# Performance work log

Hardware: AMD Instinct MI355X
Metric: run time of the kernel (lower is better)

The kernel has to match this reference:

```python
import jax, jax.numpy as jnp
import numpy as np

EPS = 1e-5
NHEADS = 4
NLAYERS = 6

def layernorm(x, g, b):
    m = jnp.mean(x, axis=-1, keepdims=True)
    v = jnp.var(x, axis=-1, keepdims=True)
    return (x - m) * jax.lax.rsqrt(v + EPS) * g + b

def leaky_relu(x):
    return jnp.where(x >= 0, x, 0.1 * x)  # LeakyReLU(negative_slope=0.1)

def biased_mha(x, bias, mask, Wq, bq, Wk, bk, Wv, bv, Wo, bo):
    # dgl.nn.BiasedMHA: scores = (q/sqrt(dh)) k^T + bias (per-head), mask==True -> -inf
    B, N, D = x.shape
    dh = D // NHEADS
    q = (x @ Wq + bq).reshape(B, N, NHEADS, dh) * (dh ** -0.5)
    k = (x @ Wk + bk).reshape(B, N, NHEADS, dh)
    v = (x @ Wv + bv).reshape(B, N, NHEADS, dh)
    scores = jnp.einsum('bqhd,bkhd->bqkh', q, k) + bias  # [B,N,N,H]
    scores = jnp.where(mask[..., None], -jnp.inf, scores)
    w = jax.nn.softmax(scores, axis=2)  # softmax over keys
    out = jnp.einsum('bqkh,bkhd->bqhd', w, v).reshape(B, N, D)
    return out @ Wo + bo

def graphormer_forward(node_feat_new, attn_bias, deg_in_emb, deg_out_emb,
                       mlp_n_W1, mlp_n_b1, mlp_n_W2, mlp_n_b2,
                       Wq, bq, Wk, bk, Wv, bv, Wo, bo,
                       ln1_g, ln1_b, W1, b1, W2, b2, ln2_g, ln2_b,
                       mlp_out_W1, mlp_out_b1, mlp_out_W2, mlp_out_b2,
                       in_degree, out_degree, attn_mask, po_idx):
    # DegreeEncoder (directed): clamp to max_degree=8, sum of two embedding tables
    deg = deg_in_emb[jnp.clip(in_degree, 0, 8)] + deg_out_emb[jnp.clip(out_degree, 0, 8)]
    # mlp_n: Linear -> LeakyReLU(0.1) -> Linear
    h = leaky_relu(node_feat_new @ mlp_n_W1 + mlp_n_b1) @ mlp_n_W2 + mlp_n_b2
    x = h + deg
    mask = attn_mask != 0
    for i in range(NLAYERS):  # 6 GraphormerLayers, norm_first=False (post-norm)
        res = x
        a = biased_mha(x, attn_bias, mask, Wq[i], bq[i], Wk[i], bk[i], Wv[i], bv[i], Wo[i], bo[i])
        x = layernorm(res + a, ln1_g[i], ln1_b[i])
        res = x
        f = jax.nn.relu(x @ W1[i] + b1[i]) @ W2[i] + b2[i]  # FFN with ReLU
        x = layernorm(res + f, ln2_g[i], ln2_b[i])
    B = x.shape[0]
    sel = x[jnp.arange(B)[:, None], po_idx].reshape(-1, x.shape[-1])  # gather PO nodes
    return leaky_relu(sel @ mlp_out_W1 + mlp_out_b1) @ mlp_out_W2 + mlp_out_b2

def setup_inputs():
    B, N, F_IN, D, HID, P, L = 8, 1024, 64, 512, 1024, 128, 6
    key = jax.random.key(0)
    ks = jax.random.split(key, 32)
    def w(k, shape, fan_in):
        return jax.random.normal(k, shape, jnp.float32) / np.float32(np.sqrt(fan_in))
    return dict(
        node_feat_new=jax.random.normal(ks[0], (B, N, F_IN), jnp.float32),
        in_degree=jax.random.randint(ks[1], (B, N), 0, 9),
        out_degree=jax.random.randint(ks[2], (B, N), 0, 9),
        dist=jax.random.randint(ks[3], (B, N, N), 0, 6).astype(jnp.int32),
        attn_mask=jax.random.randint(ks[4], (B, N, N), 0, 2).astype(jnp.int32),
        po_idx=jax.random.randint(ks[5], (B, P), 0, N),
        attn_bias=jax.random.uniform(ks[6], (B, N, N, NHEADS), jnp.float32),
        deg_in_emb=w(ks[7], (9, D), D),
        deg_out_emb=w(ks[8], (9, D), D),
        mlp_n_W1=w(ks[9], (F_IN, D // 2), F_IN), mlp_n_b1=jnp.zeros((D // 2,), jnp.float32),
        mlp_n_W2=w(ks[10], (D // 2, D), D // 2), mlp_n_b2=jnp.zeros((D,), jnp.float32),
        Wq=w(ks[11], (L, D, D), D), bq=jnp.zeros((L, D), jnp.float32),
        Wk=w(ks[12], (L, D, D), D), bk=jnp.zeros((L, D), jnp.float32),
        Wv=w(ks[13], (L, D, D), D), bv=jnp.zeros((L, D), jnp.float32),
        Wo=w(ks[14], (L, D, D), D), bo=jnp.zeros((L, D), jnp.float32),
        ln1_g=jnp.ones((L, D), jnp.float32), ln1_b=jnp.zeros((L, D), jnp.float32),
        W1=w(ks[15], (L, D, HID), D), b1=jnp.zeros((L, HID), jnp.float32),
        W2=w(ks[16], (L, HID, D), HID), b2=jnp.zeros((L, D), jnp.float32),
        ln2_g=jnp.ones((L, D), jnp.float32), ln2_b=jnp.zeros((L, D), jnp.float32),
        mlp_out_W1=w(ks[17], (D, D // 2), D), mlp_out_b1=jnp.zeros((D // 2,), jnp.float32),
        mlp_out_W2=w(ks[18], (D // 2, 1), D // 2), mlp_out_b2=jnp.zeros((1,), jnp.float32),
    )

def reference(node_feat_new, in_degree, out_degree, dist, attn_mask, po_idx, attn_bias,
              deg_in_emb, deg_out_emb, mlp_n_W1, mlp_n_b1, mlp_n_W2, mlp_n_b2,
              Wq, bq, Wk, bk, Wv, bv, Wo, bo, ln1_g, ln1_b, W1, b1, W2, b2, ln2_g, ln2_b,
              mlp_out_W1, mlp_out_b1, mlp_out_W2, mlp_out_b2):
    del dist  # original computes spatial encoding from dist but overwrites attn_bias with rand (dead code)
    return graphormer_forward(node_feat_new, attn_bias, deg_in_emb, deg_out_emb,
                              mlp_n_W1, mlp_n_b1, mlp_n_W2, mlp_n_b2,
                              Wq, bq, Wk, bk, Wv, bv, Wo, bo,
                              ln1_g, ln1_b, W1, b1, W2, b2, ln2_g, ln2_b,
                              mlp_out_W1, mlp_out_b1, mlp_out_W2, mlp_out_b2,
                              in_degree, out_degree, attn_mask, po_idx)
```

## Files before the change

kernel.cpp:

```cpp
#include <hip/hip_runtime.h>

typedef unsigned short u16;
typedef unsigned int u32;
typedef short bf16x8 __attribute__((ext_vector_type(8)));
typedef float f32x4 __attribute__((ext_vector_type(4)));

__device__ __forceinline__ float us2f(u16 u) {
  union { unsigned int i; float f; } x; x.i = ((unsigned int)u) << 16; return x.f;
}
__device__ __forceinline__ u16 f2bf(float f) {
  union { float f; unsigned int i; } x; x.f = f;
  unsigned int i = x.i;
  return (u16)((i + 0x7FFFu + ((i >> 16) & 1u)) >> 16);
}
__device__ __forceinline__ int probe_f32(const void* p) {
  return ((const u16*)p)[0] == 0;
}
__device__ __forceinline__ float ldf(const void* p, size_t i, int f32) {
  return f32 ? ((const float*)p)[i] : us2f(((const u16*)p)[i]);
}
__device__ __forceinline__ float4 ldf4(const void* p, size_t i, int f32) {
  if (f32) return *(const float4*)((const float*)p + i);
  const ushort4 t = *(const ushort4*)((const u16*)p + i);
  return make_float4(us2f(t.x), us2f(t.y), us2f(t.z), us2f(t.w));
}

__device__ __forceinline__ void tconv(u16 (*t)[72], const void* W, size_t off,
    int K, int N, u16* dst, int k0, int n0, int f32, int tid) {
  const int rr = tid >> 2, rc = (tid & 3) * 16;
  const size_t src = off + (size_t)(k0 + rr) * N + n0 + rc;
  u16 tmp[16];
  if (f32) {
    const float* p = (const float*)W + src;
#pragma unroll
    for (int q = 0; q < 4; q++) {
      const float4 f = *(const float4*)(p + q * 4);
      tmp[q * 4 + 0] = f2bf(f.x); tmp[q * 4 + 1] = f2bf(f.y);
      tmp[q * 4 + 2] = f2bf(f.z); tmp[q * 4 + 3] = f2bf(f.w);
    }
  } else {
    const u16* p = (const u16*)W + src;
    *(bf16x8*)&tmp[0] = *(const bf16x8*)p;
    *(bf16x8*)&tmp[8] = *(const bf16x8*)(p + 8);
  }
#pragma unroll
  for (int j = 0; j < 16; j++) t[rr][rc + j] = tmp[j];
  __syncthreads();
  const int wr = tid >> 2, wc = (tid & 3) * 16;
  u16 ot[16];
#pragma unroll
  for (int j = 0; j < 16; j++) ot[j] = t[wc + j][wr];
  u16* d = dst + (size_t)(n0 + wr) * K + k0 + wc;
  *(bf16x8*)d = *(bf16x8*)&ot[0];
  *(bf16x8*)(d + 8) = *(bf16x8*)&ot[8];
}

__global__ __launch_bounds__(256) void wconv_layer(const void* __restrict__ probe,
    const void* __restrict__ Wq, const void* __restrict__ Wk,
    const void* __restrict__ Wv, const void* __restrict__ Wo,
    const void* __restrict__ W1, const void* __restrict__ W2,
    const void* __restrict__ bq, const void* __restrict__ bk,
    const void* __restrict__ bv, const void* __restrict__ bo,
    const void* __restrict__ b1, const void* __restrict__ b2,
    size_t wO, size_t w1O, size_t bO, size_t b1O, u16* __restrict__ wt) {
  const int f32 = probe_f32(probe);
  __shared__ u16 t[64][72];
  const int bid = blockIdx.x, tid = threadIdx.x;
  if (bid < 192) {
    const int src = bid / 64, tt = bid % 64;
    const void* W = src == 0 ? Wq : (src == 1 ? Wk : Wv);
    tconv(t, W, wO, 512, 512, wt + src * 262144, (tt & 7) * 64, (tt >> 3) * 64, f32, tid);
  } else if (bid < 256) {
    const int tt = bid - 192;
    tconv(t, Wo, wO, 512, 512, wt + 786432, (tt & 7) * 64, (tt >> 3) * 64, f32, tid);
  } else if (bid < 384) {
    const int tt = bid - 256;
    tconv(t, W1, w1O, 512, 1024, wt + 1048576, (tt & 7) * 64, (tt >> 3) * 64, f32, tid);
  } else if (bid < 512) {
    const int tt = bid - 384;
    tconv(t, W2, w1O, 1024, 512, wt + 1572864, (tt & 15) * 64, (tt >> 4) * 64, f32, tid);
  } else {
    for (int i = tid; i < 4608; i += 256) {
      float v;
      if (i < 1536) {
        const int s = i >> 9, c = i & 511;
        v = ldf(s == 0 ? bq : (s == 1 ? bk : bv), bO + c, f32);
      } else if (i < 2048) v = ldf(bo, bO + (i - 1536), f32);
      else if (i < 3072) v = ldf(b1, b1O + (i - 2048), f32);
      else v = ldf(b2, bO + (i - 3072), f32);
      wt[2097152 + i] = f2bf(v);
    }
  }
}

__global__ __launch_bounds__(256) void wconv_node(const void* __restrict__ probe,
    const void* __restrict__ mnW1, const void* __restrict__ mnW2,
    const void* __restrict__ mnb1, const void* __restrict__ mnb2,
    u16* __restrict__ wt) {
  const int f32 = probe_f32(probe);
  __shared__ u16 t[64][72];
  const int bid = blockIdx.x, tid = threadIdx.x;
  if (bid < 4) {
    tconv(t, mnW1, 0, 64, 256, wt, 0, bid * 64, f32, tid);
  } else if (bid < 36) {
    const int tt = bid - 4;
    tconv(t, mnW2, 0, 256, 512, wt + 16384, (tt & 3) * 64, (tt >> 2) * 64, f32, tid);
  } else {
    for (int i = tid; i < 768; i += 256) {
      const float v = (i < 256) ? ldf(mnb1, i, f32) : ldf(mnb2, i - 256, f32);
      wt[147456 + i] = f2bf(v);
    }
  }
}

template <int BN, int BK>
__global__ __launch_bounds__(256) void gemm_bt(
    const void* __restrict__ probe, const void* __restrict__ A, int a_mode,
    int lda, const u16* __restrict__ Wt, const u16* __restrict__ bias,
    const u16* __restrict__ res, void* __restrict__ C, int c_bf16, int M,
    int N, int K, int act) {
  const int in_f32 = probe_f32(probe);
  const int a_f32 = (a_mode == 2) ? in_f32 : 0;
  constexpr int NT = BN / 16;
  constexpr int KH = BK / 32;
  constexpr int LDK = BK + 8;
  constexpr int TPR = 256 / BN;
  __shared__ u16 As[2][128][LDK];
  __shared__ u16 Bt[2][BN][LDK];
  const int tid = threadIdx.x;
  const int n0 = blockIdx.x * BN, m0 = blockIdx.y * 128;
  const int wv = tid >> 6, lane = tid & 63;
  const int lk = lane & 15, quad = lane >> 4;
  const int wm = wv * 32;

  f32x4 acc[2][NT];
#pragma unroll
  for (int i = 0; i < 2; i++)
#pragma unroll
    for (int j = 0; j < NT; j++) acc[i][j] = (f32x4){0.f, 0.f, 0.f, 0.f};

  const int sar = tid >> 1, sac = (tid & 1) * (BK / 2);
  const int br = tid / TPR, bc = (tid % TPR) * 16;

  u16 abuf[BK / 2], bbuf[16];
  auto loadA = [&](int k0) {
    if (a_f32) {
      const float* ap = (const float*)A + (size_t)(m0 + sar) * lda + k0 + sac;
#pragma unroll
      for (int q = 0; q < BK / 8; q++) {
        const float4 f = *(const float4*)(ap + q * 4);
        abuf[q * 4 + 0] = f2bf(f.x); abuf[q * 4 + 1] = f2bf(f.y);
        abuf[q * 4 + 2] = f2bf(f.z); abuf[q * 4 + 3] = f2bf(f.w);
      }
    } else {
      const u16* ap = (const u16*)A + (size_t)(m0 + sar) * lda + k0 + sac;
#pragma unroll
      for (int q = 0; q < BK / 16; q++)
        *(bf16x8*)&abuf[q * 8] = *(const bf16x8*)(ap + q * 8);
    }
  };
  auto loadW = [&](int k0) {
    const u16* p = Wt + (size_t)(n0 + br) * K + k0 + bc;
    *(bf16x8*)&bbuf[0] = *(const bf16x8*)p;
    *(bf16x8*)&bbuf[8] = *(const bf16x8*)(p + 8);
  };
  auto store = [&](int bi) {
#pragma unroll
    for (int q = 0; q < BK / 16; q++)
      *(bf16x8*)&As[bi][sar][sac + q * 8] = *(bf16x8*)&abuf[q * 8];
    *(bf16x8*)&Bt[bi][br][bc] = *(bf16x8*)&bbuf[0];
    *(bf16x8*)&Bt[bi][br][bc + 8] = *(bf16x8*)&bbuf[8];
  };

  const int nk = K / BK;
  loadA(0); loadW(0); store(0);
  __syncthreads();
  for (int kt = 0; kt < nk; kt++) {
    const int cur = kt & 1;
    if (kt + 1 < nk) { loadA((kt + 1) * BK); loadW((kt + 1) * BK); }
    bf16x8 af[2][KH], bfv[NT][KH];
#pragma unroll
    for (int i = 0; i < 2; i++)
#pragma unroll
      for (int h = 0; h < KH; h++)
        af[i][h] = *(const bf16x8*)&As[cur][wm + i * 16 + lk][h * 32 + quad * 8];
#pragma unroll
    for (int j = 0; j < NT; j++)
#pragma unroll
      for (int h = 0; h < KH; h++)
        bfv[j][h] = *(const bf16x8*)&Bt[cur][j * 16 + lk][h * 32 + quad * 8];
#pragma unroll
    for (int i = 0; i < 2; i++)
#pragma unroll
      for (int j = 0; j < NT; j++)
#pragma unroll
        for (int h = 0; h < KH; h++)
          acc[i][j] = __builtin_amdgcn_mfma_f32_16x16x32_bf16(
              af[i][h], bfv[j][h], acc[i][j], 0, 0, 0);
    if (kt + 1 < nk) store(cur ^ 1);
    __syncthreads();
  }

#pragma unroll
  for (int j = 0; j < NT; j++) {
    const int col = n0 + j * 16 + lk;
    const float bb = bias ? us2f(bias[col]) : 0.f;
#pragma unroll
    for (int i = 0; i < 2; i++) {
#pragma unroll
      for (int r = 0; r < 4; r++) {
        const int row = m0 + wm + i * 16 + quad * 4 + r;
        float t = acc[i][j][r] + bb;
        if (act == 1) t = t > 0.f ? t : 0.f;
        else if (act == 2) t = t >= 0.f ? t : 0.1f * t;
        if (res) t += us2f(res[(size_t)row * N + col]);
        if (c_bf16) ((u16*)C)[(size_t)row * N + col] = f2bf(t);
        else ((float*)C)[(size_t)row * N + col] = t;
      }
    }
  }
}

__global__ __launch_bounds__(256) void deg_kernel(const void* __restrict__ probe,
    u16* __restrict__ x, const int* __restrict__ ind, const int* __restrict__ outd,
    const void* __restrict__ ein, const void* __restrict__ eout) {
  const int f32 = probe_f32(probe);
  const int r = blockIdx.x, tid = threadIdx.x;
  int a = ind[r]; a = a < 0 ? 0 : (a > 8 ? 8 : a);
  int b = outd[r]; b = b < 0 ? 0 : (b > 8 ? 8 : b);
  const size_t base = (size_t)r * 512;
  for (int c = tid; c < 512; c += 256) {
    const float v = us2f(x[base + c]) + ldf(ein, (size_t)a * 512 + c, f32) +
                    ldf(eout, (size_t)b * 512 + c, f32);
    x[base + c] = f2bf(v);
  }
}

__global__ __launch_bounds__(256) void bias_pack(const void* __restrict__ probe,
    const void* __restrict__ bias, const int* __restrict__ mask,
    u16* __restrict__ biasm) {
  const int f32 = probe_f32(probe);
  __shared__ u16 pl[4][1032];
  const int bq = blockIdx.x, t = threadIdx.x;
  const size_t rk = (size_t)bq * 1024;
  const u16 NB = f2bf(-3.0e38f);
#pragma unroll
  for (int j = 0; j < 4; j++) {
    const int k = t + j * 256;
    const int mv = mask[rk + k];
    float h0, h1, h2, h3;
    if (f32) {
      const float4 f = *(const float4*)((const float*)bias + (rk + k) * 4);
      h0 = f.x; h1 = f.y; h2 = f.z; h3 = f.w;
    } else {
      const ushort4 u = *(const ushort4*)((const u16*)bias + (rk + k) * 4);
      h0 = us2f(u.x); h1 = us2f(u.y); h2 = us2f(u.z); h3 = us2f(u.w);
    }
    pl[0][k] = mv ? NB : f2bf(h0);
    pl[1][k] = mv ? NB : f2bf(h1);
    pl[2][k] = mv ? NB : f2bf(h2);
    pl[3][k] = mv ? NB : f2bf(h3);
  }
  __syncthreads();
  const int b = bq >> 10, q = bq & 1023;
  const int p = t & 3, seg = t >> 2;
  u16* dst = biasm + (((size_t)(b * 4 + p)) << 20) + (size_t)q * 1024 + seg * 16;
  *(bf16x8*)dst = *(const bf16x8*)&pl[p][seg * 16];
  *(bf16x8*)(dst + 8) = *(const bf16x8*)&pl[p][seg * 16 + 8];
}

__global__ __launch_bounds__(256) void attn_mfma(const void* __restrict__ probe,
    const u16* __restrict__ QKV, const void* __restrict__ bias,
    const int* __restrict__ mask, u16* __restrict__ O,
    const u16* __restrict__ biasm) {
  const int f32 = probe_f32(probe);
  __shared__ u16 Kls[2][32][136];
  __shared__ u16 Vt[2][128][40];
  __shared__ u16 Pl[4][16][40];
  const int b = blockIdx.z, h = blockIdx.y, q0 = blockIdx.x * 64;
  const int tid = threadIdx.x;
  const int wv = tid >> 6, lane = tid & 63;
  const int lk = lane & 15, quad = lane >> 4;
  const float scale = 0.08838834764831845f;
  const float NEG = -3.0e38f;

  const size_t qg = (size_t)(b * 1024 + q0 + wv * 16);
  const int lq = q0 + wv * 16;
  const u16* bm = biasm ? biasm + (((size_t)(b * 4 + h)) << 20) : (const u16*)0;

  bf16x8 qf[4];
#pragma unroll
  for (int c = 0; c < 4; c++)
    qf[c] = *(const bf16x8*)(QKV + (qg + lk) * 1536 + h * 128 + c * 32 + quad * 8);

  f32x4 o[8];
#pragma unroll
  for (int c = 0; c < 8; c++) o[c] = (f32x4){0.f, 0.f, 0.f, 0.f};
  float m_st[4], l_st[4];
#pragma unroll
  for (int r = 0; r < 4; r++) { m_st[r] = NEG; l_st[r] = 0.f; }

  const int kp = tid & 15, dseg = tid >> 4;

  bf16x8 ka, kb2, va, vb2;
  auto loadKV = [&](int k0) {
    const size_t r0 = (size_t)(b * 1024 + k0 + 2 * kp) * 1536 + h * 128 + dseg * 8;
    ka  = *(const bf16x8*)(QKV + r0 + 512);
    kb2 = *(const bf16x8*)(QKV + r0 + 512 + 1536);
    va  = *(const bf16x8*)(QKV + r0 + 1024);
    vb2 = *(const bf16x8*)(QKV + r0 + 1024 + 1536);
  };
  auto storeKV = [&](int bi) {
    *(bf16x8*)&Kls[bi][2 * kp][dseg * 8] = ka;
    *(bf16x8*)&Kls[bi][2 * kp + 1][dseg * 8] = kb2;
#pragma unroll
    for (int i = 0; i < 8; i++) {
      const unsigned int pk =
          ((unsigned int)(u16)vb2[i] << 16) | (unsigned int)(u16)va[i];
      *(unsigned int*)&Vt[bi][dseg * 8 + i][2 * kp] = pk;
    }
  };

  loadKV(0); storeKV(0);
  __syncthreads();

  for (int kt = 0; kt < 32; kt++) {
    const int cur = kt & 1;
    const int k0 = kt * 32;
    if (kt < 31) loadKV((kt + 1) * 32);

    float bv[2][4];
    if (bm) {
#pragma unroll
      for (int kh = 0; kh < 2; kh++)
#pragma unroll
        for (int r = 0; r < 4; r++)
          bv[kh][r] =
              us2f(bm[(size_t)(lq + quad * 4 + r) * 1024 + (k0 + kh * 16 + lk)]);
    }

    f32x4 sa[2];
#pragma unroll
    for (int kh = 0; kh < 2; kh++) {
      sa[kh] = (f32x4){0.f, 0.f, 0.f, 0.f};
#pragma unroll
      for (int c = 0; c < 4; c++) {
        const bf16x8 kf = *(const bf16x8*)&Kls[cur][kh * 16 + lk][c * 32 + quad * 8];
        sa[kh] = __builtin_amdgcn_mfma_f32_16x16x32_bf16(qf[c], kf, sa[kh], 0, 0, 0);
      }
    }
    float sv[2][4];
    if (bm) {
#pragma unroll
      for (int kh = 0; kh < 2; kh++)
#pragma unroll
        for (int r = 0; r < 4; r++)
          sv[kh][r] = sa[kh][r] * scale + bv[kh][r];
    } else {
#pragma unroll
      for (int kh = 0; kh < 2; kh++)
#pragma unroll
        for (int r = 0; r < 4; r++) {
          const size_t bidx = (qg + quad * 4 + r) * 1024 + (size_t)(k0 + kh * 16 + lk);
          const float s = sa[kh][r] * scale + ldf(bias, bidx * 4 + h, f32);
          sv[kh][r] = mask[bidx] ? NEG : s;
        }
    }
#pragma unroll
    for (int r = 0; r < 4; r++) {
      float lm = fmaxf(sv[0][r], sv[1][r]);
      lm = fmaxf(lm, __shfl_xor(lm, 1));
      lm = fmaxf(lm, __shfl_xor(lm, 2));
      lm = fmaxf(lm, __shfl_xor(lm, 4));
      lm = fmaxf(lm, __shfl_xor(lm, 8));
      const float mn = fmaxf(m_st[r], lm);
      const float al = __expf(m_st[r] - mn);
      const float p0 = (sv[0][r] <= -1e37f) ? 0.f : __expf(sv[0][r] - mn);
      const float p1 = (sv[1][r] <= -1e37f) ? 0.f : __expf(sv[1][r] - mn);
      float ts = p0 + p1;
      ts += __shfl_xor(ts, 1);
      ts += __shfl_xor(ts, 2);
      ts += __shfl_xor(ts, 4);
      ts += __shfl_xor(ts, 8);
      m_st[r] = mn;
      l_st[r] = l_st[r] * al + ts;
      Pl[wv][quad * 4 + r][lk] = f2bf(p0);
      Pl[wv][quad * 4 + r][16 + lk] = f2bf(p1);
#pragma unroll
      for (int c = 0; c < 8; c++) o[c][r] *= al;
    }
    const bf16x8 pa = *(const bf16x8*)&Pl[wv][lk][quad * 8];
#pragma unroll
    for (int c = 0; c < 8; c++) {
      const bf16x8 vf = *(const bf16x8*)&Vt[cur][c * 16 + lk][quad * 8];
      o[c] = __builtin_amdgcn_mfma_f32_16x16x32_bf16(pa, vf, o[c], 0, 0, 0);
    }
    if (kt < 31) storeKV(cur ^ 1);
    __syncthreads();
  }
#pragma unroll
  for (int r = 0; r < 4; r++) {
    const float invl = 1.f / fmaxf(l_st[r], 1e-20f);
    u16* op = O + (qg + quad * 4 + r) * 1536 + h * 128;
#pragma unroll
    for (int c = 0; c < 8; c++) op[c * 16 + lk] = f2bf(o[c][r] * invl);
  }
}

__global__ __launch_bounds__(256) void ln_kernel(const void* __restrict__ probe,
    const u16* __restrict__ in, const void* __restrict__ g,
    const void* __restrict__ bta, size_t gOff, u16* __restrict__ out) {
  const int f32 = probe_f32(probe);
  const int lane = threadIdx.x & 63, w = threadIdx.x >> 6;
  const size_t r = (size_t)blockIdx.x * 4 + w;
  const size_t base = r * 512 + lane * 8;
  const bf16x8 v = *(const bf16x8*)(in + base);
  float xv[8];
  float s = 0.f, sq = 0.f;
#pragma unroll
  for (int i = 0; i < 8; i++) {
    xv[i] = us2f((u16)v[i]);
    s += xv[i]; sq += xv[i] * xv[i];
  }
#pragma unroll
  for (int off = 32; off > 0; off >>= 1) {
    s += __shfl_xor(s, off);
    sq += __shfl_xor(sq, off);
  }
  const float m = s * (1.f / 512.f);
  const float var = fmaxf(sq * (1.f / 512.f) - m * m, 0.f);
  const float rs = rsqrtf(var + 1e-5f);
  const float4 g0 = ldf4(g, gOff + lane * 8, f32);
  const float4 g1 = ldf4(g, gOff + lane * 8 + 4, f32);
  const float4 b0 = ldf4(bta, gOff + lane * 8, f32);
  const float4 b1 = ldf4(bta, gOff + lane * 8 + 4, f32);
  const float gg[8] = {g0.x, g0.y, g0.z, g0.w, g1.x, g1.y, g1.z, g1.w};
  const float bb[8] = {b0.x, b0.y, b0.z, b0.w, b1.x, b1.y, b1.z, b1.w};
  bf16x8 ov;
#pragma unroll
  for (int i = 0; i < 8; i++) ov[i] = (short)f2bf((xv[i] - m) * rs * gg[i] + bb[i]);
  *(bf16x8*)(out + base) = ov;
}

__global__ __launch_bounds__(256) void final_kernel(const void* __restrict__ probe,
    const u16* __restrict__ x, const int* __restrict__ po,
    const void* __restrict__ W1, const void* __restrict__ b1,
    const void* __restrict__ W2, const void* __restrict__ b2,
    void* __restrict__ out) {
  const int f32 = probe_f32(probe);
  __shared__ float rsr[512];
  __shared__ float red[256];
  const int r = blockIdx.x, tid = threadIdx.x;
  const int b = r >> 7, p = r & 127;
  int n = po[b * 128 + p]; n = n < 0 ? 0 : (n > 1023 ? 1023 : n);
  const u16* row = x + ((size_t)(b * 1024 + n)) * 512;
  rsr[tid] = us2f(row[tid]); rsr[tid + 256] = us2f(row[tid + 256]);
  __syncthreads();
  float t = ldf(b1, tid, f32);
  for (int k = 0; k < 512; k++) t += rsr[k] * ldf(W1, (size_t)k * 256 + tid, f32);
  t = t >= 0.f ? t : 0.1f * t;
  red[tid] = t * ldf(W2, tid, f32);
  __syncthreads();
  for (int off = 128; off > 0; off >>= 1) {
    if (tid < off) red[tid] += red[tid + off];
    __syncthreads();
  }
  if (tid == 0) {
    const float v = red[0] + ldf(b2, 0, f32);
    if (f32) ((float*)out)[r] = v; else ((u16*)out)[r] = f2bf(v);
  }
}

extern "C" void kernel_launch(void* const* d_in, const int* in_sizes, int n_in,
                              void* d_out, int out_size, void* d_ws, size_t ws_size,
                              hipStream_t stream) {
  (void)in_sizes; (void)out_size;
  const int D = 512, HID = 1024, L = 6;
  const int M = 8192;

  const int sh = (n_in >= 33) ? 0 : 1;
#define IN(k) d_in[(k) - (((k) >= 4) ? sh : 0)]
  const void* nf   = IN(0);
  const int* ind   = (const int*)IN(1);
  const int* outd  = (const int*)IN(2);
  const int* amask = (const int*)IN(4);
  const int* po    = (const int*)IN(5);
  const void* abias = IN(6);
  const void* ein  = IN(7);
  const void* eout = IN(8);
  const void* mnW1 = IN(9);  const void* mnb1 = IN(10);
  const void* mnW2 = IN(11); const void* mnb2 = IN(12);
  const void* Wq = IN(13); const void* bq = IN(14);
  const void* Wk = IN(15); const void* bk = IN(16);
  const void* Wv = IN(17); const void* bv = IN(18);
  const void* Wo = IN(19); const void* bo = IN(20);
  const void* ln1g = IN(21); const void* ln1b = IN(22);
  const void* W1 = IN(23); const void* b1 = IN(24);
  const void* W2 = IN(25); const void* b2 = IN(26);
  const void* ln2g = IN(27); const void* ln2b = IN(28);
  const void* oW1 = IN(29); const void* ob1 = IN(30);
  const void* oW2 = IN(31); const void* ob2 = IN(32);
#undef IN
  const void* probe = ln1g;

  char* wsb = (char*)d_ws;
  u16* x   = (u16*)wsb;
  u16* yb  = (u16*)(wsb + ((size_t)8 << 20));
  u16* qkv = (u16*)(wsb + ((size_t)16 << 20));
  u16* wt  = (u16*)(wsb + ((size_t)40 << 20));
  u16* h1b = yb;
  u16* hidb = qkv;
  u16* biasm = (ws_size >= ((size_t)109 << 20))
                   ? (u16*)(wsb + ((size_t)45 << 20)) : (u16*)0;

  dim3 blk(256);
  if (biasm) bias_pack<<<8192, blk, 0, stream>>>(probe, abias, amask, biasm);
  wconv_node<<<37, blk, 0, stream>>>(probe, mnW1, mnW2, mnb1, mnb2, wt);
  gemm_bt<64, 64><<<dim3(4, M / 128), blk, 0, stream>>>(probe, nf, 2, 64, wt, wt + 147456, nullptr, h1b, 1, M, 256, 64, 2);
  gemm_bt<64, 64><<<dim3(8, M / 128), blk, 0, stream>>>(probe, h1b, 1, 256, wt + 16384, wt + 147456 + 256, nullptr, x, 1, M, D, 256, 0);
  deg_kernel<<<M, blk, 0, stream>>>(probe, x, ind, outd, ein, eout);

  for (int l = 0; l < L; l++) {
    const size_t wO = (size_t)l * D * D, bO = (size_t)l * D;
    const size_t w1O = (size_t)l * D * HID, b1O = (size_t)l * HID;
    wconv_layer<<<513, blk, 0, stream>>>(probe, Wq, Wk, Wv, Wo, W1, W2,
                                         bq, bk, bv, bo, b1, b2, wO, w1O, bO, b1O, wt);
    gemm_bt<128, 32><<<dim3(12, M / 128), blk, 0, stream>>>(probe, x, 1, 512, wt, wt + 2097152, nullptr, qkv, 1, M, 1536, 512, 0);
    attn_mfma<<<dim3(16, 4, 8), blk, 0, stream>>>(probe, qkv, abias, amask, qkv, biasm);
    gemm_bt<64, 64><<<dim3(8, M / 128), blk, 0, stream>>>(probe, qkv, 1, 1536, wt + 786432, wt + 2097152 + 1536, x, yb, 1, M, D, D, 0);
    ln_kernel<<<M / 4, blk, 0, stream>>>(probe, yb, ln1g, ln1b, bO, x);
    gemm_bt<128, 32><<<dim3(8, M / 128), blk, 0, stream>>>(probe, x, 1, 512, wt + 1048576, wt + 2097152 + 2048, nullptr, hidb, 1, M, HID, 512, 1);
    gemm_bt<64, 64><<<dim3(8, M / 128), blk, 0, stream>>>(probe, hidb, 1, 1024, wt + 1572864, wt + 2097152 + 3072, x, yb, 1, M, D, HID, 0);
    ln_kernel<<<M / 4, blk, 0, stream>>>(probe, yb, ln2g, ln2b, bO, x);
  }
  final_kernel<<<1024, blk, 0, stream>>>(probe, x, po, oW1, ob1, oW2, ob2, d_out);
}
```

Before: 1.625 ms.

## Add direct global-to-LDS GEMM kernel and use it for bf16 GEMMs

Adds a new GEMM kernel that stages A and weight tiles straight from global memory into LDS with the global_load_lds builtin (16 bytes per lane), double-buffered with BK=32. All bf16-input GEMMs in the layer loop and the second node-MLP GEMM use it in place of the register-staged gemm_bt. This drops the register round trip and the probe/f32 branching from tile loading, in exchange for unpadded LDS rows, which may cause bank conflicts on fragment reads, and a single-barrier pipeline.

```diff
diff --git a/kernel.cpp b/kernel.cpp
--- a/kernel.cpp
+++ b/kernel.cpp
@@ -5,6 +5,9 @@
 typedef short bf16x8 __attribute__((ext_vector_type(8)));
 typedef float f32x4 __attribute__((ext_vector_type(4)));
 
+typedef const u32 __attribute__((address_space(1))) glb_u32;
+typedef u32 __attribute__((address_space(3))) lds_u32;
+
 __device__ __forceinline__ float us2f(u16 u) {
   union { unsigned int i; float f; } x; x.i = ((unsigned int)u) << 16; return x.f;
 }
@@ -23,6 +26,9 @@
   if (f32) return *(const float4*)((const float*)p + i);
   const ushort4 t = *(const ushort4*)((const u16*)p + i);
   return make_float4(us2f(t.x), us2f(t.y), us2f(t.z), us2f(t.w));
+}
+__device__ __forceinline__ void gld16(const u16* g, u16* l) {
+  __builtin_amdgcn_global_load_lds((glb_u32*)g, (lds_u32*)l, 16, 0, 0);
 }
 
 __device__ __forceinline__ void tconv(u16 (*t)[72], const void* W, size_t off,
@@ -113,6 +119,83 @@
   }
 }
 
+template <int BN>
+__global__ __launch_bounds__(256) void gemm_gld(
+    const u16* __restrict__ A, int lda, const u16* __restrict__ Wt,
+    const u16* __restrict__ bias, const u16* __restrict__ res,
+    void* __restrict__ C, int c_bf16, int M, int N, int K, int act) {
+  constexpr int NT = BN / 16;
+  constexpr int BISS = BN / 64;
+  __shared__ u16 As[2][128][32];
+  __shared__ u16 Bs[2][BN][32];
+  const int tid = threadIdx.x;
+  const int n0 = blockIdx.x * BN, m0 = blockIdx.y * 128;
+  const int wv = tid >> 6, lane = tid & 63;
+  const int lk = lane & 15, quad = lane >> 4;
+  const int wm = wv * 32;
+  const int srow = lane >> 2, scol = (lane & 3) * 8;
+
+  f32x4 acc[2][NT];
+#pragma unroll
+  for (int i = 0; i < 2; i++)
+#pragma unroll
+    for (int j = 0; j < NT; j++) acc[i][j] = (f32x4){0.f, 0.f, 0.f, 0.f};
+
+  auto stage = [&](int bi, int k0) {
+#pragma unroll
+    for (int j = 0; j < 2; j++) {
+      const int r0 = wv * 32 + j * 16;
+      gld16(A + (size_t)(m0 + r0 + srow) * lda + k0 + scol, &As[bi][r0][0]);
+    }
+#pragma unroll
+    for (int j = 0; j < BISS; j++) {
+      const int r0 = wv * (BN / 4) + j * 16;
+      gld16(Wt + (size_t)(n0 + r0 + srow) * K + k0 + scol, &Bs[bi][r0][0]);
+    }
+  };
+
+  const int nk = K >> 5;
+  stage(0, 0);
+  __syncthreads();
+  for (int kt = 0; kt < nk; kt++) {
+    const int cur = kt & 1;
+    if (kt + 1 < nk) stage(cur ^ 1, (kt + 1) * 32);
+    bf16x8 af[2], bfv[NT];
+#pragma unroll
+    for (int i = 0; i < 2; i++)
+      af[i] = *(const bf16x8*)&As[cur][wm + i * 16 + lk][quad * 8];
+#pragma unroll
+    for (int j = 0; j < NT; j++)
+      bfv[j] = *(const bf16x8*)&Bs[cur][j * 16 + lk][quad * 8];
+#pragma unroll
+    for (int i = 0; i < 2; i++)
+#pragma unroll
+      for (int j = 0; j < NT; j++)
+        acc[i][j] = __builtin_amdgcn_mfma_f32_16x16x32_bf16(af[i], bfv[j],
+                                                            acc[i][j], 0, 0, 0);
+    __syncthreads();
+  }
+
+#pragma unroll
+  for (int j = 0; j < NT; j++) {
+    const int col = n0 + j * 16 + lk;
+    const float bb = bias ? us2f(bias[col]) : 0.f;
+#pragma unroll
+    for (int i = 0; i < 2; i++) {
+#pragma unroll
+      for (int r = 0; r < 4; r++) {
+        const int row = m0 + wm + i * 16 + quad * 4 + r;
+        float t = acc[i][j][r] + bb;
+        if (act == 1) t = t > 0.f ? t : 0.f;
+        else if (act == 2) t = t >= 0.f ? t : 0.1f * t;
+        if (res) t += us2f(res[(size_t)row * N + col]);
+        if (c_bf16) ((u16*)C)[(size_t)row * N + col] = f2bf(t);
+        else ((float*)C)[(size_t)row * N + col] = t;
+      }
+    }
+  }
+}
+
 template <int BN, int BK>
 __global__ __launch_bounds__(256) void gemm_bt(
     const void* __restrict__ probe, const void* __restrict__ A, int a_mode,
@@ -517,7 +600,7 @@
   if (biasm) bias_pack<<<8192, blk, 0, stream>>>(probe, abias, amask, biasm);
   wconv_node<<<37, blk, 0, stream>>>(probe, mnW1, mnW2, mnb1, mnb2, wt);
   gemm_bt<64, 64><<<dim3(4, M / 128), blk, 0, stream>>>(probe, nf, 2, 64, wt, wt + 147456, nullptr, h1b, 1, M, 256, 64, 2);
-  gemm_bt<64, 64><<<dim3(8, M / 128), blk, 0, stream>>>(probe, h1b, 1, 256, wt + 16384, wt + 147456 + 256, nullptr, x, 1, M, D, 256, 0);
+  gemm_gld<64><<<dim3(8, M / 128), blk, 0, stream>>>(h1b, 256, wt + 16384, wt + 147456 + 256, nullptr, x, 1, M, D, 256, 0);
   deg_kernel<<<M, blk, 0, stream>>>(probe, x, ind, outd, ein, eout);
 
   for (int l = 0; l < L; l++) {
@@ -525,12 +608,12 @@
     const size_t w1O = (size_t)l * D * HID, b1O = (size_t)l * HID;
     wconv_layer<<<513, blk, 0, stream>>>(probe, Wq, Wk, Wv, Wo, W1, W2,
                                          bq, bk, bv, bo, b1, b2, wO, w1O, bO, b1O, wt);
-    gemm_bt<128, 32><<<dim3(12, M / 128), blk, 0, stream>>>(probe, x, 1, 512, wt, wt + 2097152, nullptr, qkv, 1, M, 1536, 512, 0);
+    gemm_gld<128><<<dim3(12, M / 128), blk, 0, stream>>>(x, 512, wt, wt + 2097152, nullptr, qkv, 1, M, 1536, 512, 0);
     attn_mfma<<<dim3(16, 4, 8), blk, 0, stream>>>(probe, qkv, abias, amask, qkv, biasm);
-    gemm_bt<64, 64><<<dim3(8, M / 128), blk, 0, stream>>>(probe, qkv, 1, 1536, wt + 786432, wt + 2097152 + 1536, x, yb, 1, M, D, D, 0);
+    gemm_gld<64><<<dim3(8, M / 128), blk, 0, stream>>>(qkv, 1536, wt + 786432, wt + 2097152 + 1536, x, yb, 1, M, D, D, 0);
     ln_kernel<<<M / 4, blk, 0, stream>>>(probe, yb, ln1g, ln1b, bO, x);
-    gemm_bt<128, 32><<<dim3(8, M / 128), blk, 0, stream>>>(probe, x, 1, 512, wt + 1048576, wt + 2097152 + 2048, nullptr, hidb, 1, M, HID, 512, 1);
-    gemm_bt<64, 64><<<dim3(8, M / 128), blk, 0, stream>>>(probe, hidb, 1, 1024, wt + 1572864, wt + 2097152 + 3072, x, yb, 1, M, D, HID, 0);
+    gemm_gld<128><<<dim3(8, M / 128), blk, 0, stream>>>(x, 512, wt + 1048576, wt + 2097152 + 2048, nullptr, hidb, 1, M, HID, 512, 1);
+    gemm_gld<64><<<dim3(8, M / 128), blk, 0, stream>>>(hidb, 1024, wt + 1572864, wt + 2097152 + 3072, x, yb, 1, M, D, HID, 0);
     ln_kernel<<<M / 4, blk, 0, stream>>>(probe, yb, ln2g, ln2b, bO, x);
   }
   final_kernel<<<1024, blk, 0, stream>>>(probe, x, po, oW1, ob1, oW2, ob2, d_out);
```

Result: no change. 1.629 ms (+0.3%).
